# Kernel tuning notes

Hardware: AMD Instinct MI355X
Metric: run time of the kernel (lower is better)

## Reference

```python
import jax, jax.numpy as jnp
import numpy as np

N = 100000   # nodes
E = 1600000  # edges (avg degree 16)
B = 64       # graphs in batch
D_IN = 64
D = 64       # d_model


def setup_inputs() -> dict:
    key = jax.random.key(0)
    ks = jax.random.split(key, 12)
    inp = {}
    inp["x_raw"] = jax.random.normal(ks[0], (N, D_IN), dtype=jnp.float32)
    inp["edge_index"] = jax.random.randint(ks[1], (2, E), 0, N)
    inp["batch"] = jnp.sort(jax.random.randint(ks[2], (N,), 0, B))
    # SAGEConv params per layer: lin_l (weight+bias, applied to neighbor mean),
    # lin_r (weight only, applied to root) -- PyG defaults.
    dins = [D_IN, D, D]
    for i, din in enumerate(dins):
        scale = 1.0 / np.sqrt(din)
        inp[f"Wl{i}"] = jax.random.normal(ks[3 + 3 * i], (D, din), dtype=jnp.float32) * scale
        inp[f"bl{i}"] = jnp.zeros((D,), dtype=jnp.float32)
        inp[f"Wr{i}"] = jax.random.normal(ks[4 + 3 * i], (D, din), dtype=jnp.float32) * scale
    return inp


def _sage_conv(x, src, dst, Wl, bl, Wr):
    """PyG SAGEConv(normalize=True): mean-aggregate neighbors, lin_l + lin_r, L2 norm."""
    msg = jax.ops.segment_sum(x[src], dst, num_segments=N)          # [N, d_in]
    deg = jax.ops.segment_sum(jnp.ones((src.shape[0],), x.dtype), dst, num_segments=N)
    mean = msg / jnp.maximum(deg, 1.0)[:, None]
    out = mean @ Wl.T + bl + x @ Wr.T                               # [N, D]
    nrm = jnp.sqrt(jnp.sum(out * out, axis=-1, keepdims=True))
    return out / jnp.maximum(nrm, 1e-12)


def reference(x_raw, edge_index, batch, Wl0, bl0, Wr0, Wl1, bl1, Wr1, Wl2, bl2, Wr2):
    src, dst = edge_index[0], edge_index[1]
    # dropout is identity in eval mode
    h = jax.nn.relu(_sage_conv(x_raw, src, dst, Wl0, bl0, Wr0))
    h = jax.nn.relu(_sage_conv(h, src, dst, Wl1, bl1, Wr1))
    h = jax.nn.relu(_sage_conv(h, src, dst, Wl2, bl2, Wr2))
    # readout='sum': scatter-sum over batch ids -> [B, D]
    return jax.ops.segment_sum(h, batch, num_segments=B)
```

## Files before the change

### kernel.cpp

```cpp
#include <hip/hip_runtime.h>

#define DFEAT 64

typedef __attribute__((ext_vector_type(8))) short bf16x8;
typedef __attribute__((ext_vector_type(4))) float f32x4;

__device__ __forceinline__ float bfhi(unsigned int u) {
    return __builtin_bit_cast(float, u & 0xFFFF0000u);
}
__device__ __forceinline__ float bflo(unsigned int u) {
    return __builtin_bit_cast(float, u << 16);
}
__device__ __forceinline__ unsigned short f2bf(float f) {
    unsigned int u = __builtin_bit_cast(unsigned int, f);
    u += 0x7FFFu + ((u >> 16) & 1u);
    return (unsigned short)(u >> 16);
}

__global__ void __launch_bounds__(256)
cvt_bf16_kernel(const float* __restrict__ in, unsigned short* __restrict__ outb,
                int n4) {
    int i = blockIdx.x * 256 + threadIdx.x;
    if (i >= n4) return;
    const float4 v = reinterpret_cast<const float4*>(in)[i];
    uint2 p;
    p.x = (unsigned int)f2bf(v.x) | ((unsigned int)f2bf(v.y) << 16);
    p.y = (unsigned int)f2bf(v.z) | ((unsigned int)f2bf(v.w) << 16);
    reinterpret_cast<uint2*>(outb)[i] = p;
}

__global__ void __launch_bounds__(256)
wfrag_cvt_kernel(const float* __restrict__ Wl, const float* __restrict__ Wr,
                 unsigned short* __restrict__ wfrag) {
    const int i4 = blockIdx.x * 256 + threadIdx.x;
    if (i4 >= 1024) return;
    const float4 wl = reinterpret_cast<const float4*>(Wl)[i4];
    const float4 wr = reinterpret_cast<const float4*>(Wr)[i4];
    const int feat = i4 >> 4;
    const int n = feat >> 4, cc = feat & 15;
    const int k0 = (i4 & 15) << 2;
    const int qq = (k0 >> 3) & 3, tl = k0 >> 5, j0 = k0 & 7;
    const int lofs = (qq * 16 + cc) * 8 + j0;
    uint2 pl, pr;
    pl.x = (unsigned int)f2bf(wl.x) | ((unsigned int)f2bf(wl.y) << 16);
    pl.y = (unsigned int)f2bf(wl.z) | ((unsigned int)f2bf(wl.w) << 16);
    pr.x = (unsigned int)f2bf(wr.x) | ((unsigned int)f2bf(wr.y) << 16);
    pr.y = (unsigned int)f2bf(wr.z) | ((unsigned int)f2bf(wr.w) << 16);
    *reinterpret_cast<uint2*>(&wfrag[(n * 4 + tl) * 512 + lofs]) = pl;
    *reinterpret_cast<uint2*>(&wfrag[(n * 4 + 2 + tl) * 512 + lofs]) = pr;
}


__global__ void __launch_bounds__(256)
bucket_hist_kernel(const int* __restrict__ dsts, int* __restrict__ bhist, int E) {
    __shared__ int h[512];
    const int tid = threadIdx.x;
    h[tid] = 0; h[tid + 256] = 0;
    __syncthreads();
    for (int e = blockIdx.x * 256 + tid; e < E; e += gridDim.x * 256)
        atomicAdd(&h[dsts[e] >> 8], 1);
    __syncthreads();
    for (int b = tid; b < 512; b += 256)
        if (h[b]) atomicAdd(&bhist[b], h[b]);
}

__global__ void __launch_bounds__(256)
bucket_scan_kernel(const int* __restrict__ bhist, int* __restrict__ bbase,
                   int* __restrict__ bcur) {
    __shared__ int sm[512];
    const int tid = threadIdx.x;
    sm[tid] = bhist[tid]; sm[tid + 256] = bhist[tid + 256];
    __syncthreads();
    for (int s = 1; s < 512; s <<= 1) {
        int a0 = (tid >= s) ? sm[tid - s] : 0;
        int a1 = sm[tid + 256 - s];
        __syncthreads();
        sm[tid] += a0; sm[tid + 256] += a1;
        __syncthreads();
    }
    for (int b = tid; b < 512; b += 256) {
        int excl = b ? sm[b - 1] : 0;
        bbase[b] = excl; bcur[b] = excl;
    }
    if (tid == 0) bbase[512] = sm[511];
}

#define BIN_CH 2048
__global__ void __launch_bounds__(256)
bin_kernel(const int* __restrict__ srcs, const int* __restrict__ dsts,
           int* __restrict__ bcur, unsigned int* __restrict__ pairbuf, int E) {
    __shared__ int hist[512];
    __shared__ int sscan[512];
    __shared__ int gbase[512];
    __shared__ unsigned int staged[BIN_CH];
    __shared__ unsigned short sbkt[BIN_CH];

    const int tid = threadIdx.x;
    const int base = blockIdx.x * BIN_CH;
    const int chcnt = min(BIN_CH, E - base);

    hist[tid] = 0; hist[tid + 256] = 0;
    __syncthreads();

    unsigned int pk[8];
    unsigned short bb[8], rr[8];
#pragma unroll
    for (int k = 0; k < 8; ++k) {
        int i = k * 256 + tid;
        if (i < chcnt) {
            int e = base + i;
            int d = dsts[e];
            int s = srcs[e];
            int b = d >> 8;
            int r = atomicAdd(&hist[b], 1);
            pk[k] = ((unsigned int)(d & 255) << 24) | (unsigned int)s;
            bb[k] = (unsigned short)b;
            rr[k] = (unsigned short)r;
        } else {
            bb[k] = 0xFFFFu;
        }
    }
    __syncthreads();

    sscan[tid] = hist[tid]; sscan[tid + 256] = hist[tid + 256];
    __syncthreads();
    for (int s = 1; s < 512; s <<= 1) {
        int a0 = (tid >= s) ? sscan[tid - s] : 0;
        int a1 = sscan[tid + 256 - s];
        __syncthreads();
        sscan[tid] += a0; sscan[tid + 256] += a1;
        __syncthreads();
    }

    for (int b = tid; b < 512; b += 256) {
        int c = hist[b];
        gbase[b] = c ? atomicAdd(&bcur[b], c) : 0;
    }
    __syncthreads();

#pragma unroll
    for (int k = 0; k < 8; ++k) {
        if (bb[k] != 0xFFFFu) {
            int b = bb[k];
            int lpos = (b ? sscan[b - 1] : 0) + rr[k];
            staged[lpos] = pk[k];
            sbkt[lpos] = (unsigned short)b;
        }
    }
    __syncthreads();

    for (int i = tid; i < chcnt; i += 256) {
        int b = sbkt[i];
        int excl = b ? sscan[b - 1] : 0;
        pairbuf[gbase[b] + (i - excl)] = staged[i];
    }
}

__global__ void __launch_bounds__(256)
bucket_fill_kernel(const unsigned int* __restrict__ pairbuf,
                   const int* __restrict__ bbase,
                   int* __restrict__ rowptr, int* __restrict__ col,
                   int N, int E) {
    __shared__ int hist[256];
    __shared__ int scan_[256];
    __shared__ int cur[256];

    const int tid = threadIdx.x;
    const int b = blockIdx.x;
    const int node0 = b << 8;
    const int bb0 = bbase[b];
    const int cnt = bbase[b + 1] - bb0;

    hist[tid] = 0;
    __syncthreads();
    for (int i = tid; i < cnt; i += 256)
        atomicAdd(&hist[pairbuf[bb0 + i] >> 24], 1);
    __syncthreads();

    scan_[tid] = hist[tid];
    __syncthreads();
    for (int s = 1; s < 256; s <<= 1) {
        int a = (tid >= s) ? scan_[tid - s] : 0;
        __syncthreads();
        scan_[tid] += a;
        __syncthreads();
    }
    int excl = tid ? scan_[tid - 1] : 0;
    if (node0 + tid < N) rowptr[node0 + tid] = bb0 + excl;
    if (b == 0 && tid == 0) rowptr[N] = E;
    cur[tid] = bb0 + excl;
    __syncthreads();

    for (int i = tid; i < cnt; i += 256) {
        unsigned int p = pairbuf[bb0 + i];
        int pos = atomicAdd(&cur[p >> 24], 1);
        col[pos] = (int)(p & 0xFFFFFFu);
    }
}

__global__ void __launch_bounds__(256, 8)
fused_sage_kernel(const unsigned short* __restrict__ xb,
                  const int* __restrict__ rowptr, const int* __restrict__ col,
                  const unsigned short* __restrict__ wfrag,
                  const float* __restrict__ bl,
                  unsigned short* __restrict__ h_out,
                  const int* __restrict__ batch, float* __restrict__ out,
                  int n_nodes, int final_layer) {
    const int tid = threadIdx.x;
    const int tiles = (n_nodes + 15) >> 4;
    const int tile = blockIdx.x * 4 + (tid >> 6);
    if (tile >= tiles) return;

    const int lane = tid & 63;
    const int c = lane & 15;
    const int q = lane >> 4;

    const int base = tile << 4;
    const bool valid = (base + c) < n_nodes;
    const int node = valid ? (base + c) : (n_nodes - 1);

    const uint4* rows4 = reinterpret_cast<const uint4*>(xb);
    const int st = rowptr[node];
    const int deg = valid ? (rowptr[node + 1] - st) : 0;

    float accA[8], accB[8];
#pragma unroll
    for (int j = 0; j < 8; ++j) { accA[j] = 0.f; accB[j] = 0.f; }

    if (deg > 0) {
        const int dm1 = deg - 1;
        const int* cp = col + st;
        int c0 = cp[0];
        uint4 a0 = rows4[(size_t)c0 * 8 + q];
        uint4 b0 = rows4[(size_t)c0 * 8 + 4 + q];
        int c1 = cp[min(1, dm1)];
        for (int j = 0; j < deg; ++j) {
            const int c2 = cp[min(j + 2, dm1)];
            const uint4 a1 = rows4[(size_t)c1 * 8 + q];
            const uint4 b1 = rows4[(size_t)c1 * 8 + 4 + q];
            accA[0] += bflo(a0.x); accA[1] += bfhi(a0.x);
            accA[2] += bflo(a0.y); accA[3] += bfhi(a0.y);
            accA[4] += bflo(a0.z); accA[5] += bfhi(a0.z);
            accA[6] += bflo(a0.w); accA[7] += bfhi(a0.w);
            accB[0] += bflo(b0.x); accB[1] += bfhi(b0.x);
            accB[2] += bflo(b0.y); accB[3] += bfhi(b0.y);
            accB[4] += bflo(b0.z); accB[5] += bfhi(b0.z);
            accB[6] += bflo(b0.w); accB[7] += bfhi(b0.w);
            a0 = a1; b0 = b1; c1 = c2;
        }
    }

    const float inv = (deg > 0) ? (1.0f / (float)deg) : 0.0f;
    bf16x8 F0, F1;
#pragma unroll
    for (int j = 0; j < 8; ++j) {
        F0[j] = (short)f2bf(accA[j] * inv);
        F1[j] = (short)f2bf(accB[j] * inv);
    }
    const uint4* xrow = reinterpret_cast<const uint4*>(&xb[(size_t)node * 64]);
    const bf16x8 F2 = __builtin_bit_cast(bf16x8, xrow[q]);
    const bf16x8 F3 = __builtin_bit_cast(bf16x8, xrow[4 + q]);

    const bf16x8* fragp = reinterpret_cast<const bf16x8*>(wfrag);
    f32x4 acc[4];
#pragma unroll
    for (int n = 0; n < 4; ++n) acc[n] = (f32x4){0.f, 0.f, 0.f, 0.f};

#pragma unroll
    for (int n = 0; n < 4; ++n) {
        bf16x8 w0 = fragp[(n * 4 + 0) * 64 + lane];
        bf16x8 w1 = fragp[(n * 4 + 1) * 64 + lane];
        bf16x8 w2 = fragp[(n * 4 + 2) * 64 + lane];
        bf16x8 w3 = fragp[(n * 4 + 3) * 64 + lane];
        acc[n] = __builtin_amdgcn_mfma_f32_16x16x32_bf16(w0, F0, acc[n], 0, 0, 0);
        acc[n] = __builtin_amdgcn_mfma_f32_16x16x32_bf16(w1, F1, acc[n], 0, 0, 0);
        acc[n] = __builtin_amdgcn_mfma_f32_16x16x32_bf16(w2, F2, acc[n], 0, 0, 0);
        acc[n] = __builtin_amdgcn_mfma_f32_16x16x32_bf16(w3, F3, acc[n], 0, 0, 0);
    }

    float v[4][4];
    float ss = 0.f;
#pragma unroll
    for (int n = 0; n < 4; ++n) {
        const float4 b4 = reinterpret_cast<const float4*>(bl)[n * 4 + q];
        v[n][0] = acc[n][0] + b4.x;
        v[n][1] = acc[n][1] + b4.y;
        v[n][2] = acc[n][2] + b4.z;
        v[n][3] = acc[n][3] + b4.w;
#pragma unroll
        for (int r = 0; r < 4; ++r) ss += v[n][r] * v[n][r];
    }
    ss += __shfl_xor(ss, 16, 64);
    ss += __shfl_xor(ss, 32, 64);
    const float nrm = 1.0f / fmaxf(sqrtf(ss), 1e-12f);

    if (!final_layer) {
        if (valid) {
            uint2* dst = reinterpret_cast<uint2*>(&h_out[(size_t)(base + c) * 64]);
#pragma unroll
            for (int n = 0; n < 4; ++n) {
                float o0 = fmaxf(v[n][0] * nrm, 0.f), o1 = fmaxf(v[n][1] * nrm, 0.f);
                float o2 = fmaxf(v[n][2] * nrm, 0.f), o3 = fmaxf(v[n][3] * nrm, 0.f);
                uint2 p;
                p.x = (unsigned int)f2bf(o0) | ((unsigned int)f2bf(o1) << 16);
                p.y = (unsigned int)f2bf(o2) | ((unsigned int)f2bf(o3) << 16);
                dst[n * 4 + q] = p;
            }
        }
    } else {
        float o[4][4];
#pragma unroll
        for (int n = 0; n < 4; ++n)
#pragma unroll
            for (int r = 0; r < 4; ++r)
                o[n][r] = valid ? fmaxf(v[n][r] * nrm, 0.f) : 0.f;

        const int lastn = min(base + 15, n_nodes - 1);
        const int gb0 = batch[base];
        if (gb0 == batch[lastn]) {
#pragma unroll
            for (int n = 0; n < 4; ++n)
#pragma unroll
                for (int r = 0; r < 4; ++r) {
                    float s = o[n][r];
                    s += __shfl_xor(s, 1, 64);
                    s += __shfl_xor(s, 2, 64);
                    s += __shfl_xor(s, 4, 64);
                    s += __shfl_xor(s, 8, 64);
                    if (c == 0)
                        atomicAdd(&out[(size_t)gb0 * DFEAT + n * 16 + q * 4 + r], s);
                }
        } else {
            if (valid) {
                const int gb = batch[base + c];
#pragma unroll
                for (int n = 0; n < 4; ++n)
#pragma unroll
                    for (int r = 0; r < 4; ++r)
                        atomicAdd(&out[(size_t)gb * DFEAT + n * 16 + q * 4 + r], o[n][r]);
            }
        }
    }
}

extern "C" void kernel_launch(void* const* d_in, const int* in_sizes, int n_in,
                              void* d_out, int out_size, void* d_ws, size_t ws_size,
                              hipStream_t stream) {
    const float* x_raw = (const float*)d_in[0];
    const int*   eidx  = (const int*)d_in[1];
    const int*   batch = (const int*)d_in[2];
    const float* Wl0 = (const float*)d_in[3];
    const float* bl0 = (const float*)d_in[4];
    const float* Wr0 = (const float*)d_in[5];
    const float* Wl1 = (const float*)d_in[6];
    const float* bl1 = (const float*)d_in[7];
    const float* Wr1 = (const float*)d_in[8];
    const float* Wl2 = (const float*)d_in[9];
    const float* bl2 = (const float*)d_in[10];
    const float* Wr2 = (const float*)d_in[11];

    const int N = in_sizes[0] / DFEAT;
    const int E = in_sizes[1] / 2;
    const int* srcs = eidx;
    const int* dsts = eidx + E;
    float* out = (float*)d_out;

    const int NB = (N + 255) >> 8;

    char* ws = (char*)d_ws;
    auto align512 = [](size_t v) { return (v + 511) & ~(size_t)511; };
    size_t off = 0;
    int* rowptr = (int*)(ws + off); off += align512(((size_t)N + 1) * 4);
    int* col    = (int*)(ws + off); off += align512((size_t)E * 4);
    int* bhist  = (int*)(ws + off); off += align512(512 * 4);
    int* bbase  = (int*)(ws + off); off += align512(513 * 4);
    int* bcur   = (int*)(ws + off); off += align512(512 * 4);
    unsigned short* wfrag0 = (unsigned short*)(ws + off); off += align512(8192 * 2);
    unsigned short* wfrag1 = (unsigned short*)(ws + off); off += align512(8192 * 2);
    unsigned short* wfrag2 = (unsigned short*)(ws + off); off += align512(8192 * 2);
    unsigned short* xb = (unsigned short*)(ws + off); off += align512((size_t)N * DFEAT * 2);
    unsigned short* hA = (unsigned short*)(ws + off); off += align512((size_t)N * DFEAT * 2);
    unsigned short* hB = (unsigned short*)(ws + off);
    unsigned int* pairbuf = (unsigned int*)hA;

    hipMemsetAsync(bhist, 0, 512 * 4, stream);
    hipMemsetAsync(out, 0, (size_t)out_size * 4, stream);

    const int n4 = N * DFEAT / 4;
    cvt_bf16_kernel<<<(n4 + 255) / 256, 256, 0, stream>>>(x_raw, xb, n4);
    wfrag_cvt_kernel<<<4, 256, 0, stream>>>(Wl0, Wr0, wfrag0);
    wfrag_cvt_kernel<<<4, 256, 0, stream>>>(Wl1, Wr1, wfrag1);
    wfrag_cvt_kernel<<<4, 256, 0, stream>>>(Wl2, Wr2, wfrag2);

    bucket_hist_kernel<<<512, 256, 0, stream>>>(dsts, bhist, E);
    bucket_scan_kernel<<<1, 256, 0, stream>>>(bhist, bbase, bcur);
    bin_kernel<<<(E + BIN_CH - 1) / BIN_CH, 256, 0, stream>>>(srcs, dsts, bcur, pairbuf, E);
    bucket_fill_kernel<<<NB, 256, 0, stream>>>(pairbuf, bbase, rowptr, col, N, E);

    const int tiles    = (N + 15) / 16;
    const int xfBlocks = (tiles + 3) / 4;

    fused_sage_kernel<<<xfBlocks, 256, 0, stream>>>(xb, rowptr, col, wfrag0, bl0,
                                                    hA, nullptr, nullptr, N, 0);
    fused_sage_kernel<<<xfBlocks, 256, 0, stream>>>(hA, rowptr, col, wfrag1, bl1,
                                                    hB, nullptr, nullptr, N, 0);
    fused_sage_kernel<<<xfBlocks, 256, 0, stream>>>(hB, rowptr, col, wfrag2, bl2,
                                                    nullptr, batch, out, N, 1);
}
```

Before: 322.6 us.

## Permute nodes by graph and descending degree to balance wave work

```diff
diff --git a/kernel.cpp b/kernel.cpp
--- a/kernel.cpp
+++ b/kernel.cpp
@@ -1,6 +1,7 @@
 #include <hip/hip_runtime.h>
 
 #define DFEAT 64
+#define NKEY 16384
 
 typedef __attribute__((ext_vector_type(8))) short bf16x8;
 typedef __attribute__((ext_vector_type(4))) float f32x4;
@@ -198,9 +199,51 @@
     }
 }
 
+__global__ void __launch_bounds__(256)
+key_hist_kernel(const int* __restrict__ rowptr, const int* __restrict__ batch,
+                int* __restrict__ khist, int* __restrict__ keyarr, int N) {
+    int n = blockIdx.x * 256 + threadIdx.x;
+    if (n >= N) return;
+    int deg = rowptr[n + 1] - rowptr[n];
+    int k = batch[n] * 256 + (255 - min(deg, 255));
+    keyarr[n] = k;
+    atomicAdd(&khist[k], 1);
+}
+
+__global__ void __launch_bounds__(1024)
+key_scan_kernel(const int* __restrict__ khist, int* __restrict__ kcur) {
+    __shared__ int tsum[1024];
+    const int t = threadIdx.x;
+    int loc[16];
+    int s = 0;
+#pragma unroll
+    for (int i = 0; i < 16; ++i) { loc[i] = s; s += khist[t * 16 + i]; }
+    tsum[t] = s;
+    __syncthreads();
+    for (int st = 1; st < 1024; st <<= 1) {
+        int a = (t >= st) ? tsum[t - st] : 0;
+        __syncthreads();
+        tsum[t] += a;
+        __syncthreads();
+    }
+    const int excl = t ? tsum[t - 1] : 0;
+#pragma unroll
+    for (int i = 0; i < 16; ++i) kcur[t * 16 + i] = excl + loc[i];
+}
+
+__global__ void __launch_bounds__(256)
+key_scatter_kernel(const int* __restrict__ keyarr, int* __restrict__ kcur,
+                   int* __restrict__ nodeperm, int N) {
+    int n = blockIdx.x * 256 + threadIdx.x;
+    if (n >= N) return;
+    int pos = atomicAdd(&kcur[keyarr[n]], 1);
+    nodeperm[pos] = n;
+}
+
 __global__ void __launch_bounds__(256, 8)
 fused_sage_kernel(const unsigned short* __restrict__ xb,
                   const int* __restrict__ rowptr, const int* __restrict__ col,
+                  const int* __restrict__ nodeperm,
                   const unsigned short* __restrict__ wfrag,
                   const float* __restrict__ bl,
                   unsigned short* __restrict__ h_out,
@@ -216,8 +259,9 @@
     const int q = lane >> 4;
 
     const int base = tile << 4;
-    const bool valid = (base + c) < n_nodes;
-    const int node = valid ? (base + c) : (n_nodes - 1);
+    const int slot = base + c;
+    const bool valid = slot < n_nodes;
+    const int node = nodeperm[valid ? slot : (n_nodes - 1)];
 
     const uint4* rows4 = reinterpret_cast<const uint4*>(xb);
     const int st = rowptr[node];
@@ -296,7 +340,7 @@
 
     if (!final_layer) {
         if (valid) {
-            uint2* dst = reinterpret_cast<uint2*>(&h_out[(size_t)(base + c) * 64]);
+            uint2* dst = reinterpret_cast<uint2*>(&h_out[(size_t)node * 64]);
 #pragma unroll
             for (int n = 0; n < 4; ++n) {
                 float o0 = fmaxf(v[n][0] * nrm, 0.f), o1 = fmaxf(v[n][1] * nrm, 0.f);
@@ -315,9 +359,9 @@
             for (int r = 0; r < 4; ++r)
                 o[n][r] = valid ? fmaxf(v[n][r] * nrm, 0.f) : 0.f;
 
-        const int lastn = min(base + 15, n_nodes - 1);
-        const int gb0 = batch[base];
-        if (gb0 == batch[lastn]) {
+        const int gb0 = batch[nodeperm[base]];
+        const int gbL = batch[nodeperm[min(base + 15, n_nodes - 1)]];
+        if (gb0 == gbL) {
 #pragma unroll
             for (int n = 0; n < 4; ++n)
 #pragma unroll
@@ -332,7 +376,7 @@
                 }
         } else {
             if (valid) {
-                const int gb = batch[base + c];
+                const int gb = batch[node];
 #pragma unroll
                 for (int n = 0; n < 4; ++n)
 #pragma unroll
@@ -375,6 +419,10 @@
     int* bhist  = (int*)(ws + off); off += align512(512 * 4);
     int* bbase  = (int*)(ws + off); off += align512(513 * 4);
     int* bcur   = (int*)(ws + off); off += align512(512 * 4);
+    int* khist  = (int*)(ws + off); off += align512((size_t)NKEY * 4);
+    int* kcur   = (int*)(ws + off); off += align512((size_t)NKEY * 4);
+    int* keyarr = (int*)(ws + off); off += align512((size_t)N * 4);
+    int* nodeperm = (int*)(ws + off); off += align512((size_t)N * 4);
     unsigned short* wfrag0 = (unsigned short*)(ws + off); off += align512(8192 * 2);
     unsigned short* wfrag1 = (unsigned short*)(ws + off); off += align512(8192 * 2);
     unsigned short* wfrag2 = (unsigned short*)(ws + off); off += align512(8192 * 2);
@@ -384,6 +432,7 @@
     unsigned int* pairbuf = (unsigned int*)hA;
 
     hipMemsetAsync(bhist, 0, 512 * 4, stream);
+    hipMemsetAsync(khist, 0, (size_t)NKEY * 4, stream);
     hipMemsetAsync(out, 0, (size_t)out_size * 4, stream);
 
     const int n4 = N * DFEAT / 4;
@@ -397,13 +446,21 @@
     bin_kernel<<<(E + BIN_CH - 1) / BIN_CH, 256, 0, stream>>>(srcs, dsts, bcur, pairbuf, E);
     bucket_fill_kernel<<<NB, 256, 0, stream>>>(pairbuf, bbase, rowptr, col, N, E);
 
+    const int nblk = (N + 255) / 256;
+    key_hist_kernel<<<nblk, 256, 0, stream>>>(rowptr, batch, khist, keyarr, N);
+    key_scan_kernel<<<1, 1024, 0, stream>>>(khist, kcur);
+    key_scatter_kernel<<<nblk, 256, 0, stream>>>(keyarr, kcur, nodeperm, N);
+
     const int tiles    = (N + 15) / 16;
     const int xfBlocks = (tiles + 3) / 4;
 
-    fused_sage_kernel<<<xfBlocks, 256, 0, stream>>>(xb, rowptr, col, wfrag0, bl0,
+    fused_sage_kernel<<<xfBlocks, 256, 0, stream>>>(xb, rowptr, col, nodeperm,
+                                                    wfrag0, bl0,
                                                     hA, nullptr, nullptr, N, 0);
-    fused_sage_kernel<<<xfBlocks, 256, 0, stream>>>(hA, rowptr, col, wfrag1, bl1,
+    fused_sage_kernel<<<xfBlocks, 256, 0, stream>>>(hA, rowptr, col, nodeperm,
+                                                    wfrag1, bl1,
                                                     hB, nullptr, nullptr, N, 0);
-    fused_sage_kernel<<<xfBlocks, 256, 0, stream>>>(hB, rowptr, col, wfrag2, bl2,
+    fused_sage_kernel<<<xfBlocks, 256, 0, stream>>>(hB, rowptr, col, nodeperm,
+                                                    wfrag2, bl2,
                                                     nullptr, batch, out, N, 1);
 }
```

Measured after the change: 367.4 us. +13.9%, slower.
